# Optimization experiments

Measured on AMD Instinct MI355X. Metric: run time of the kernel, lower is better.

The kernel has to match this reference:

```python
import jax, jax.numpy as jnp
import numpy as np

N, IN_DIM, HID, HEAD = 32768, 512, 512, 4
E = 524288


def setup_inputs() -> dict:
    key = jax.random.key(0)
    ks = jax.random.split(key, 12)
    s_in = 1.0 / np.sqrt(IN_DIM)
    s_h = 1.0 / np.sqrt(HID)
    s_c = 1.0 / np.sqrt(HID * HEAD)
    s_f = 1.0 / np.sqrt(HID * 2)
    return {
        "x": jax.random.normal(ks[0], (N, IN_DIM), jnp.float32),
        "inter_h": jax.random.normal(ks[1], (N, IN_DIM), jnp.float32),
        "edge_index": jax.random.randint(ks[2], (2, E), 0, N, jnp.int64),
        "batch": jnp.zeros((N,), jnp.int64),
        # per-head projection weights stored [HEAD, in, out] (x @ W)
        "Wq": jax.random.uniform(ks[3], (HEAD, IN_DIM, HID), jnp.float32, -s_in, s_in),
        "Wk": jax.random.uniform(ks[4], (HEAD, IN_DIM, HID), jnp.float32, -s_in, s_in),
        "Wv": jax.random.uniform(ks[5], (HEAD, IN_DIM, HID), jnp.float32, -s_in, s_in),
        "Wc": jax.random.uniform(ks[6], (HID * HEAD, HID), jnp.float32, -s_c, s_c),
        "W1": jax.random.uniform(ks[7], (HID, HID * 2), jnp.float32, -s_h, s_h),
        "b1": jax.random.uniform(ks[8], (HID * 2,), jnp.float32, -s_h, s_h),
        "W2": jax.random.uniform(ks[9], (HID * 2, HID), jnp.float32, -s_f, s_f),
        "b2": jax.random.uniform(ks[10], (HID,), jnp.float32, -s_f, s_f),
        "ln_g": jnp.ones((HID,), jnp.float32),
        "ln_b": jnp.zeros((HID,), jnp.float32),
    }


def _layernorm(h, g, b, eps=1e-5):
    mu = jnp.mean(h, axis=-1, keepdims=True)
    var = jnp.mean(jnp.square(h - mu), axis=-1, keepdims=True)
    return (h - mu) * jax.lax.rsqrt(var + eps) * g + b


def reference(x, inter_h, edge_index, batch, Wq, Wk, Wv, Wc, W1, b1, W2, b2, ln_g, ln_b):
    # edge_index and batch are unused by the original forward.
    q = jnp.einsum("ni,hio->nho", x, Wq)        # [N, H, D]
    k = jnp.einsum("ni,hio->nho", inter_h, Wk)  # [N, H, D]
    v = jnp.einsum("ni,hio->nho", x, Wv)        # [N, H, D]
    scale = 1.0 / jnp.sqrt(jnp.float32(HID))
    att = jnp.sum(q * k, axis=-1) * scale       # [N, H]
    alpha = jax.nn.softmax(att, axis=0)         # softmax over nodes (dim 0)
    tp = v * alpha[:, :, None]                  # [N, H, D]
    mo = tp.reshape(tp.shape[0], HEAD * HID)    # head-major concat, matches torch.cat(dim=1)
    mo = mo @ Wc                                # [N, D]
    h1 = _layernorm(mo + x, ln_g, ln_b)
    ff = jnp.maximum(h1 @ W1 + b1, 0.0) @ W2 + b2
    return _layernorm(ff + h1, ln_g, ln_b)
```

## Files before the change

kernel.cpp:

```cpp
#include <hip/hip_runtime.h>

typedef unsigned short u16;
typedef short short8 __attribute__((ext_vector_type(8)));
typedef unsigned short ushort8 __attribute__((ext_vector_type(8)));
typedef float f32x4 __attribute__((ext_vector_type(4)));

#define NN 32768L

__device__ __forceinline__ u16 f2bf(float f) {
  unsigned u = __float_as_uint(f);
  u += 0x7FFFu + ((u >> 16) & 1u);
  return (u16)(u >> 16);
}
__device__ __forceinline__ float bf2f(u16 u) {
  return __uint_as_float(((unsigned)u) << 16);
}

__global__ __launch_bounds__(256) void fill_f32_k(float* __restrict__ out, long n, float v) {
  long i = (long)blockIdx.x * 256 + threadIdx.x;
  if (i < n) out[i] = v;
}

__global__ __launch_bounds__(256) void cast_bf16_k(const float* __restrict__ in,
                                                   u16* __restrict__ out, long n) {
  long i = ((long)blockIdx.x * 256 + threadIdx.x) * 8;
  if (i >= n) return;
  const float4* p = (const float4*)(in + i);
  float4 a = p[0], b = p[1];
  ushort8 r;
  r[0] = f2bf(a.x); r[1] = f2bf(a.y); r[2] = f2bf(a.z); r[3] = f2bf(a.w);
  r[4] = f2bf(b.x); r[5] = f2bf(b.y); r[6] = f2bf(b.z); r[7] = f2bf(b.w);
  *(ushort8*)(out + i) = r;
}

__global__ __launch_bounds__(256) void transpose_cast(const float* __restrict__ in,
                                                      u16* __restrict__ out, int R, int C) {
  __shared__ float t[32][33];
  int c0 = blockIdx.x * 32, r0 = blockIdx.y * 32;
  int tx = threadIdx.x, ty = threadIdx.y;
#pragma unroll
  for (int j = 0; j < 32; j += 8)
    t[ty + j][tx] = in[(long)(r0 + ty + j) * C + c0 + tx];
  __syncthreads();
#pragma unroll
  for (int j = 0; j < 32; j += 8)
    out[(long)(c0 + ty + j) * R + r0 + tx] = f2bf(t[tx][ty + j]);
}

template <int EPI>
__global__ __launch_bounds__(256) void gemm_bt(const u16* __restrict__ A,
                                               const u16* __restrict__ Bt,
                                               u16* __restrict__ C, int K,
                                               int lda, int ldb, int ldc,
                                               long sA, long sB, long sC,
                                               const float* __restrict__ ep0) {
  __shared__ u16 As[4096];
  __shared__ u16 Bs[4096];
  const int tid = threadIdx.x;
  const int wid = tid >> 6, lane = tid & 63;
  const int bx = blockIdx.x, by = blockIdx.y, bz = blockIdx.z;
  const u16* Ab = A + bz * sA + (long)by * 128 * lda;
  const u16* Bb = Bt + bz * sB + (long)bx * 128 * ldb;
  const int e0 = tid * 8;
  const int ar = e0 >> 5, ac = e0 & 31;
  const int r15 = lane & 15, kg = lane >> 4;
  const int wrow = (wid >> 1) * 64, wcol = (wid & 1) * 64;

  f32x4 acc[4][4];
  const f32x4 z4 = {0.f, 0.f, 0.f, 0.f};
#pragma unroll
  for (int mi = 0; mi < 4; ++mi)
#pragma unroll
    for (int ni = 0; ni < 4; ++ni) acc[mi][ni] = z4;

  for (int k0 = 0; k0 < K; k0 += 32) {
    short8 a0 = *(const short8*)(Ab + (long)ar * lda + k0 + ac);
    short8 a1 = *(const short8*)(Ab + (long)(ar + 64) * lda + k0 + ac);
    short8 b0 = *(const short8*)(Bb + (long)ar * ldb + k0 + ac);
    short8 b1 = *(const short8*)(Bb + (long)(ar + 64) * ldb + k0 + ac);
    *(short8*)(As + e0) = a0;
    *(short8*)(As + e0 + 2048) = a1;
    *(short8*)(Bs + e0) = b0;
    *(short8*)(Bs + e0 + 2048) = b1;
    __syncthreads();
    short8 af[4], bfr[4];
#pragma unroll
    for (int mi = 0; mi < 4; ++mi)
      af[mi] = *(const short8*)(As + (wrow + mi * 16 + r15) * 32 + kg * 8);
#pragma unroll
    for (int ni = 0; ni < 4; ++ni)
      bfr[ni] = *(const short8*)(Bs + (wcol + ni * 16 + r15) * 32 + kg * 8);
#pragma unroll
    for (int mi = 0; mi < 4; ++mi)
#pragma unroll
      for (int ni = 0; ni < 4; ++ni)
        acc[mi][ni] =
            __builtin_amdgcn_mfma_f32_16x16x32_bf16(af[mi], bfr[ni], acc[mi][ni], 0, 0, 0);
    __syncthreads();
  }

  u16* Cp = C + bz * sC;
  const long crow0 = (long)by * 128 + wrow;
  const int ccol0 = bx * 128 + wcol;
#pragma unroll
  for (int mi = 0; mi < 4; ++mi) {
#pragma unroll
    for (int ni = 0; ni < 4; ++ni) {
      const int gc = ccol0 + ni * 16 + r15;
#pragma unroll
      for (int r = 0; r < 4; ++r) {
        const long gr = crow0 + mi * 16 + kg * 4 + r;
        float v = acc[mi][ni][r];
        if (EPI == 1) { v += ep0[gc]; v = fmaxf(v, 0.f); }
        if (EPI == 2) { v += ep0[gc]; }
        Cp[gr * ldc + gc] = f2bf(v);
      }
    }
  }
}

__global__ __launch_bounds__(256) void att_dot_k(const float* __restrict__ x,
                                                 const u16* __restrict__ zb,
                                                 float* __restrict__ att) {
  int wid = threadIdx.x >> 6, lane = threadIdx.x & 63;
  long n = (long)blockIdx.x * 4 + wid;
  const float4* xp = (const float4*)(x + n * 512 + lane * 8);
  float4 x0 = xp[0], x1 = xp[1];
  float xf[8] = {x0.x, x0.y, x0.z, x0.w, x1.x, x1.y, x1.z, x1.w};
  const float scale = 0.044194173824159216f;
#pragma unroll
  for (int h = 0; h < 4; ++h) {
    ushort8 zv = *(const ushort8*)(zb + n * 2048 + h * 512 + lane * 8);
    float s = 0.f;
#pragma unroll
    for (int j = 0; j < 8; ++j) s += xf[j] * bf2f(zv[j]);
#pragma unroll
    for (int o = 32; o; o >>= 1) s += __shfl_xor(s, o);
    if (lane == 0) att[n * 4 + h] = s * scale;
  }
}

__global__ __launch_bounds__(1024) void softmax_k(const float* __restrict__ att,
                                                  float* __restrict__ alpha) {
  int h = blockIdx.x;
  int tid = threadIdx.x;
  __shared__ float red[16];
  float lm = -1e30f;
  for (long i = tid; i < NN; i += 1024) lm = fmaxf(lm, att[i * 4 + h]);
#pragma unroll
  for (int o = 32; o; o >>= 1) lm = fmaxf(lm, __shfl_xor(lm, o));
  if ((tid & 63) == 0) red[tid >> 6] = lm;
  __syncthreads();
  float gm = red[0];
  for (int i = 1; i < 16; ++i) gm = fmaxf(gm, red[i]);
  __syncthreads();
  float ls = 0.f;
  for (long i = tid; i < NN; i += 1024) ls += __expf(att[i * 4 + h] - gm);
#pragma unroll
  for (int o = 32; o; o >>= 1) ls += __shfl_xor(ls, o);
  if ((tid & 63) == 0) red[tid >> 6] = ls;
  __syncthreads();
  float gs = 0.f;
  for (int i = 0; i < 16; ++i) gs += red[i];
  float inv = 1.0f / gs;
  for (long i = tid; i < NN; i += 1024)
    alpha[i * 4 + h] = __expf(att[i * 4 + h] - gm) * inv;
}

__global__ __launch_bounds__(256) void ascale_k(const float* __restrict__ x,
                                                const float* __restrict__ alpha,
                                                u16* __restrict__ out, long row0) {
  long e = ((long)blockIdx.x * 256 + threadIdx.x) * 8;
  long r = e >> 11;
  int c = (int)(e & 2047);
  int h = c >> 9;
  float al = alpha[(row0 + r) * 4 + h];
  const float4* xp = (const float4*)(x + (row0 + r) * 512 + (c & 511));
  float4 x0 = xp[0], x1 = xp[1];
  ushort8 o;
  o[0] = f2bf(al * x0.x); o[1] = f2bf(al * x0.y);
  o[2] = f2bf(al * x0.z); o[3] = f2bf(al * x0.w);
  o[4] = f2bf(al * x1.x); o[5] = f2bf(al * x1.y);
  o[6] = f2bf(al * x1.z); o[7] = f2bf(al * x1.w);
  *(ushort8*)(out + e) = o;
}

template <int RBF, int OUTF>
__global__ __launch_bounds__(256) void ln_k(const u16* __restrict__ a,
                                            const void* __restrict__ resid,
                                            const float* __restrict__ g,
                                            const float* __restrict__ b,
                                            void* __restrict__ out) {
  int wid = threadIdx.x >> 6, lane = threadIdx.x & 63;
  long row = (long)blockIdx.x * 4 + wid;
  ushort8 av = *(const ushort8*)(a + row * 512 + lane * 8);
  float v[8];
  if (RBF) {
    ushort8 rv = *(const ushort8*)((const u16*)resid + row * 512 + lane * 8);
#pragma unroll
    for (int j = 0; j < 8; ++j) v[j] = bf2f(av[j]) + bf2f(rv[j]);
  } else {
    const float4* rp = (const float4*)((const float*)resid + row * 512 + lane * 8);
    float4 r0 = rp[0], r1 = rp[1];
    float rr[8] = {r0.x, r0.y, r0.z, r0.w, r1.x, r1.y, r1.z, r1.w};
#pragma unroll
    for (int j = 0; j < 8; ++j) v[j] = bf2f(av[j]) + rr[j];
  }
  float s = 0.f, q = 0.f;
#pragma unroll
  for (int j = 0; j < 8; ++j) { s += v[j]; q += v[j] * v[j]; }
#pragma unroll
  for (int o = 32; o; o >>= 1) { s += __shfl_xor(s, o); q += __shfl_xor(q, o); }
  float mu = s * (1.0f / 512.0f);
  float var = q * (1.0f / 512.0f) - mu * mu;
  float rs = rsqrtf(var + 1e-5f);
  const float4* gp = (const float4*)(g + lane * 8);
  const float4* bp = (const float4*)(b + lane * 8);
  float4 g0 = gp[0], g1 = gp[1], b0 = bp[0], b1 = bp[1];
  float gg[8] = {g0.x, g0.y, g0.z, g0.w, g1.x, g1.y, g1.z, g1.w};
  float bb[8] = {b0.x, b0.y, b0.z, b0.w, b1.x, b1.y, b1.z, b1.w};
  float o_[8];
#pragma unroll
  for (int j = 0; j < 8; ++j) o_[j] = (v[j] - mu) * rs * gg[j] + bb[j];
  if (OUTF) {
    float4 q0 = {o_[0], o_[1], o_[2], o_[3]}, q1 = {o_[4], o_[5], o_[6], o_[7]};
    float4* op = (float4*)((float*)out + row * 512 + lane * 8);
    op[0] = q0;
    op[1] = q1;
  } else {
    ushort8 r;
#pragma unroll
    for (int j = 0; j < 8; ++j) r[j] = f2bf(o_[j]);
    *(ushort8*)((u16*)out + row * 512 + lane * 8) = r;
  }
}

extern "C" void kernel_launch(void* const* d_in, const int* in_sizes, int n_in,
                              void* d_out, int out_size, void* d_ws, size_t ws_size,
                              hipStream_t stream) {
  static const int EXPS[14] = {16777216, 16777216, 1048576, 32768, 1048576, 1048576,
                               1048576,  1048576,  524288,  1024,  524288,  512,
                               512,      512};
  float sv = 0.f;
  if (n_in != 14) {
    sv = 390.f;
  } else {
    for (int i = 0; i < 14; ++i)
      if (in_sizes[i] != EXPS[i]) { sv = 200.f + 10.f * i; break; }
  }
  if (sv == 0.f && out_size != 16777216) sv = 400.f;
  if (sv == 0.f && ws_size < 116391936UL) sv = 500.f + (float)(ws_size >> 24);
  if (sv != 0.f) {
    fill_f32_k<<<65536, 256, 0, stream>>>((float*)d_out, 16777216L, sv);
    return;
  }

  const float* x   = (const float*)d_in[0];
  const float* ih  = (const float*)d_in[1];
  const float* Wq  = (const float*)d_in[4];
  const float* Wk  = (const float*)d_in[5];
  const float* Wv  = (const float*)d_in[6];
  const float* Wc  = (const float*)d_in[7];
  const float* W1  = (const float*)d_in[8];
  const float* b1  = (const float*)d_in[9];
  const float* W2  = (const float*)d_in[10];
  const float* b2  = (const float*)d_in[11];
  const float* lng = (const float*)d_in[12];
  const float* lnb = (const float*)d_in[13];

  char* w = (char*)d_ws;
  u16* yb   = (u16*)(w + 0L);
  u16* apc  = (u16*)(w + 0L);
  u16* f1c  = (u16*)(w + 0L);
  u16* zc   = (u16*)(w + 33554432L);
  u16* moc  = (u16*)(w + 33554432L);
  u16* g2   = (u16*)(w + 33554432L);
  u16* h1   = (u16*)(w + 67108864L);
  char* wb  = w + 100663296L;
  u16* Wqb  = (u16*)(wb + 0L);
  u16* Wkb  = (u16*)(wb + 2097152L);
  u16* Wvb  = (u16*)(wb + 4194304L);
  u16* Wct  = (u16*)(wb + 6291456L);
  u16* Mcat = (u16*)(wb + 8388608L);
  u16* Pt   = (u16*)(wb + 10485760L);
  u16* W1t  = (u16*)(wb + 12582912L);
  u16* W2t  = (u16*)(wb + 13631488L);
  float* att   = (float*)(wb + 14680064L);
  float* alpha = (float*)(wb + 15204352L);

  dim3 b256(256);

  cast_bf16_k<<<8192, b256, 0, stream>>>(ih, yb, 16777216L);
  cast_bf16_k<<<512, b256, 0, stream>>>(Wq, Wqb, 1048576L);
  cast_bf16_k<<<512, b256, 0, stream>>>(Wk, Wkb, 1048576L);
  cast_bf16_k<<<512, b256, 0, stream>>>(Wv, Wvb, 1048576L);
  transpose_cast<<<dim3(16, 64), dim3(32, 8), 0, stream>>>(Wc, Wct, 2048, 512);
  transpose_cast<<<dim3(32, 16), dim3(32, 8), 0, stream>>>(W1, W1t, 512, 1024);
  transpose_cast<<<dim3(16, 32), dim3(32, 8), 0, stream>>>(W2, W2t, 1024, 512);

  gemm_bt<0><<<dim3(4, 4, 4), b256, 0, stream>>>(Wqb, Wkb, Mcat, 512, 512, 512, 512,
                                                 262144L, 262144L, 262144L, nullptr);
  gemm_bt<0><<<dim3(4, 4, 4), b256, 0, stream>>>(Wct, Wvb, Pt, 512, 2048, 512, 2048,
                                                 512L, 262144L, 512L, nullptr);

  for (int c = 0; c < 8; ++c) {
    long r0 = (long)c * 4096;
    gemm_bt<0><<<dim3(16, 32), b256, 0, stream>>>(yb + r0 * 512, Mcat, zc, 512,
                                                  512, 512, 2048, 0L, 0L, 0L, nullptr);
    att_dot_k<<<1024, b256, 0, stream>>>(x + r0 * 512, zc, att + r0 * 4);
  }
  softmax_k<<<4, 1024, 0, stream>>>(att, alpha);

  for (int c = 0; c < 4; ++c) {
    long r0 = (long)c * 8192;
    ascale_k<<<8192, b256, 0, stream>>>(x, alpha, apc, r0);
    gemm_bt<0><<<dim3(4, 64), b256, 0, stream>>>(apc, Pt, moc, 2048,
                                                 2048, 2048, 512, 0L, 0L, 0L, nullptr);
    ln_k<0, 0><<<2048, b256, 0, stream>>>(moc, x + r0 * 512, lng, lnb, h1 + r0 * 512);
  }

  for (int c = 0; c < 4; ++c) {
    long r0 = (long)c * 8192;
    gemm_bt<1><<<dim3(8, 64), b256, 0, stream>>>(h1 + r0 * 512, W1t, f1c, 512,
                                                 512, 512, 1024, 0L, 0L, 0L, b1);
    gemm_bt<2><<<dim3(4, 64), b256, 0, stream>>>(f1c, W2t, g2 + r0 * 512, 1024,
                                                 1024, 1024, 512, 0L, 0L, 0L, b2);
  }

  ln_k<1, 1><<<8192, b256, 0, stream>>>(g2, h1, lng, lnb, d_out);
}
```

Baseline: 932.7 us.

## Fuse attention dot and alpha scaling into GEMMs, drop row chunking

The attention-score dot product is folded into the epilogue of the z GEMM, which reduces across lanes and accumulates per-head scores with atomicAdd, so the bf16 z intermediate is never written out. The alpha-times-x bf16 operand is built on the fly in the A-load of the Wc GEMM, which removes the separate ascale kernel and its buffer. The chunked launch loops are replaced by single full-size launches, and the workspace is enlarged to hold full-size intermediates. In exchange the code adds atomics, a zero-fill of the score buffer, and fp32 x loads and conversion inside the GEMM inner loop, which may slow that loop.

After: 764.5 us. 1.22x faster.

```diff
diff --git a/kernel.cpp b/kernel.cpp
--- a/kernel.cpp
+++ b/kernel.cpp
@@ -47,13 +47,15 @@
     out[(long)(c0 + ty + j) * R + r0 + tx] = f2bf(t[tx][ty + j]);
 }
 
-template <int EPI>
+template <int EPI, int ASRC>
 __global__ __launch_bounds__(256) void gemm_bt(const u16* __restrict__ A,
                                                const u16* __restrict__ Bt,
-                                               u16* __restrict__ C, int K,
+                                               void* __restrict__ C, int K,
                                                int lda, int ldb, int ldc,
                                                long sA, long sB, long sC,
-                                               const float* __restrict__ ep0) {
+                                               const float* __restrict__ ep0,
+                                               const float* __restrict__ xf,
+                                               const float* __restrict__ alf) {
   __shared__ u16 As[4096];
   __shared__ u16 Bs[4096];
   const int tid = threadIdx.x;
@@ -74,8 +76,27 @@
     for (int ni = 0; ni < 4; ++ni) acc[mi][ni] = z4;
 
   for (int k0 = 0; k0 < K; k0 += 32) {
-    short8 a0 = *(const short8*)(Ab + (long)ar * lda + k0 + ac);
-    short8 a1 = *(const short8*)(Ab + (long)(ar + 64) * lda + k0 + ac);
+    short8 a0, a1;
+    if (ASRC == 0) {
+      a0 = *(const short8*)(Ab + (long)ar * lda + k0 + ac);
+      a1 = *(const short8*)(Ab + (long)(ar + 64) * lda + k0 + ac);
+    } else {
+      const int hh = (k0 + ac) >> 9, cc = (k0 + ac) & 511;
+      const long r0a = (long)by * 128 + ar;
+      const float al0 = alf[r0a * 4 + hh];
+      const float al1 = alf[(r0a + 64) * 4 + hh];
+      const float4* p0 = (const float4*)(xf + r0a * 512 + cc);
+      const float4* p1 = (const float4*)(xf + (r0a + 64) * 512 + cc);
+      float4 u0 = p0[0], u1 = p0[1], v0 = p1[0], v1 = p1[1];
+      a0[0] = (short)f2bf(al0 * u0.x); a0[1] = (short)f2bf(al0 * u0.y);
+      a0[2] = (short)f2bf(al0 * u0.z); a0[3] = (short)f2bf(al0 * u0.w);
+      a0[4] = (short)f2bf(al0 * u1.x); a0[5] = (short)f2bf(al0 * u1.y);
+      a0[6] = (short)f2bf(al0 * u1.z); a0[7] = (short)f2bf(al0 * u1.w);
+      a1[0] = (short)f2bf(al1 * v0.x); a1[1] = (short)f2bf(al1 * v0.y);
+      a1[2] = (short)f2bf(al1 * v0.z); a1[3] = (short)f2bf(al1 * v0.w);
+      a1[4] = (short)f2bf(al1 * v1.x); a1[5] = (short)f2bf(al1 * v1.y);
+      a1[6] = (short)f2bf(al1 * v1.z); a1[7] = (short)f2bf(al1 * v1.w);
+    }
     short8 b0 = *(const short8*)(Bb + (long)ar * ldb + k0 + ac);
     short8 b1 = *(const short8*)(Bb + (long)(ar + 64) * ldb + k0 + ac);
     *(short8*)(As + e0) = a0;
@@ -99,9 +120,32 @@
     __syncthreads();
   }
 
-  u16* Cp = C + bz * sC;
   const long crow0 = (long)by * 128 + wrow;
   const int ccol0 = bx * 128 + wcol;
+
+  if (EPI == 3) {
+    const int hh = ccol0 >> 9;
+    const int cb = (ccol0 & 511) + r15;
+    float* att = (float*)C;
+    const float scale = 0.044194173824159216f;
+#pragma unroll
+    for (int mi = 0; mi < 4; ++mi) {
+#pragma unroll
+      for (int r = 0; r < 4; ++r) {
+        const long gr = crow0 + mi * 16 + kg * 4 + r;
+        float p = 0.f;
+#pragma unroll
+        for (int ni = 0; ni < 4; ++ni)
+          p += acc[mi][ni][r] * xf[gr * 512 + cb + ni * 16];
+        p += __shfl_xor(p, 1); p += __shfl_xor(p, 2);
+        p += __shfl_xor(p, 4); p += __shfl_xor(p, 8);
+        if (r15 == 0) atomicAdd(att + gr * 4 + hh, p * scale);
+      }
+    }
+    return;
+  }
+
+  u16* Cp = (u16*)C + bz * sC;
 #pragma unroll
   for (int mi = 0; mi < 4; ++mi) {
 #pragma unroll
@@ -119,27 +163,6 @@
   }
 }
 
-__global__ __launch_bounds__(256) void att_dot_k(const float* __restrict__ x,
-                                                 const u16* __restrict__ zb,
-                                                 float* __restrict__ att) {
-  int wid = threadIdx.x >> 6, lane = threadIdx.x & 63;
-  long n = (long)blockIdx.x * 4 + wid;
-  const float4* xp = (const float4*)(x + n * 512 + lane * 8);
-  float4 x0 = xp[0], x1 = xp[1];
-  float xf[8] = {x0.x, x0.y, x0.z, x0.w, x1.x, x1.y, x1.z, x1.w};
-  const float scale = 0.044194173824159216f;
-#pragma unroll
-  for (int h = 0; h < 4; ++h) {
-    ushort8 zv = *(const ushort8*)(zb + n * 2048 + h * 512 + lane * 8);
-    float s = 0.f;
-#pragma unroll
-    for (int j = 0; j < 8; ++j) s += xf[j] * bf2f(zv[j]);
-#pragma unroll
-    for (int o = 32; o; o >>= 1) s += __shfl_xor(s, o);
-    if (lane == 0) att[n * 4 + h] = s * scale;
-  }
-}
-
 __global__ __launch_bounds__(1024) void softmax_k(const float* __restrict__ att,
                                                   float* __restrict__ alpha) {
   int h = blockIdx.x;
@@ -165,24 +188,6 @@
   float inv = 1.0f / gs;
   for (long i = tid; i < NN; i += 1024)
     alpha[i * 4 + h] = __expf(att[i * 4 + h] - gm) * inv;
-}
-
-__global__ __launch_bounds__(256) void ascale_k(const float* __restrict__ x,
-                                                const float* __restrict__ alpha,
-                                                u16* __restrict__ out, long row0) {
-  long e = ((long)blockIdx.x * 256 + threadIdx.x) * 8;
-  long r = e >> 11;
-  int c = (int)(e & 2047);
-  int h = c >> 9;
-  float al = alpha[(row0 + r) * 4 + h];
-  const float4* xp = (const float4*)(x + (row0 + r) * 512 + (c & 511));
-  float4 x0 = xp[0], x1 = xp[1];
-  ushort8 o;
-  o[0] = f2bf(al * x0.x); o[1] = f2bf(al * x0.y);
-  o[2] = f2bf(al * x0.z); o[3] = f2bf(al * x0.w);
-  o[4] = f2bf(al * x1.x); o[5] = f2bf(al * x1.y);
-  o[6] = f2bf(al * x1.z); o[7] = f2bf(al * x1.w);
-  *(ushort8*)(out + e) = o;
 }
 
 template <int RBF, int OUTF>
@@ -249,7 +254,7 @@
       if (in_sizes[i] != EXPS[i]) { sv = 200.f + 10.f * i; break; }
   }
   if (sv == 0.f && out_size != 16777216) sv = 400.f;
-  if (sv == 0.f && ws_size < 116391936UL) sv = 500.f + (float)(ws_size >> 24);
+  if (sv == 0.f && ws_size < 149946368UL) sv = 500.f + (float)(ws_size >> 24);
   if (sv != 0.f) {
     fill_f32_k<<<65536, 256, 0, stream>>>((float*)d_out, 16777216L, sv);
     return;
@@ -270,13 +275,11 @@
 
   char* w = (char*)d_ws;
   u16* yb   = (u16*)(w + 0L);
-  u16* apc  = (u16*)(w + 0L);
-  u16* f1c  = (u16*)(w + 0L);
-  u16* zc   = (u16*)(w + 33554432L);
-  u16* moc  = (u16*)(w + 33554432L);
-  u16* g2   = (u16*)(w + 33554432L);
-  u16* h1   = (u16*)(w + 67108864L);
-  char* wb  = w + 100663296L;
+  u16* f1   = (u16*)(w + 0L);
+  u16* moc  = (u16*)(w + 67108864L);
+  u16* g2   = (u16*)(w + 67108864L);
+  u16* h1   = (u16*)(w + 100663296L);
+  char* wb  = w + 134217728L;
   u16* Wqb  = (u16*)(wb + 0L);
   u16* Wkb  = (u16*)(wb + 2097152L);
   u16* Wvb  = (u16*)(wb + 4194304L);
@@ -297,35 +300,28 @@
   transpose_cast<<<dim3(16, 64), dim3(32, 8), 0, stream>>>(Wc, Wct, 2048, 512);
   transpose_cast<<<dim3(32, 16), dim3(32, 8), 0, stream>>>(W1, W1t, 512, 1024);
   transpose_cast<<<dim3(16, 32), dim3(32, 8), 0, stream>>>(W2, W2t, 1024, 512);
-
-  gemm_bt<0><<<dim3(4, 4, 4), b256, 0, stream>>>(Wqb, Wkb, Mcat, 512, 512, 512, 512,
-                                                 262144L, 262144L, 262144L, nullptr);
-  gemm_bt<0><<<dim3(4, 4, 4), b256, 0, stream>>>(Wct, Wvb, Pt, 512, 2048, 512, 2048,
-                                                 512L, 262144L, 512L, nullptr);
-
-  for (int c = 0; c < 8; ++c) {
-    long r0 = (long)c * 4096;
-    gemm_bt<0><<<dim3(16, 32), b256, 0, stream>>>(yb + r0 * 512, Mcat, zc, 512,
-                                                  512, 512, 2048, 0L, 0L, 0L, nullptr);
-    att_dot_k<<<1024, b256, 0, stream>>>(x + r0 * 512, zc, att + r0 * 4);
-  }
+  fill_f32_k<<<512, b256, 0, stream>>>(att, 131072L, 0.f);
+
+  gemm_bt<0, 0><<<dim3(4, 4, 4), b256, 0, stream>>>(
+      Wqb, Wkb, Mcat, 512, 512, 512, 512, 262144L, 262144L, 262144L,
+      nullptr, nullptr, nullptr);
+  gemm_bt<0, 0><<<dim3(4, 4, 4), b256, 0, stream>>>(
+      Wct, Wvb, Pt, 512, 2048, 512, 2048, 512L, 262144L, 512L,
+      nullptr, nullptr, nullptr);
+
+  gemm_bt<3, 0><<<dim3(16, 256), b256, 0, stream>>>(
+      yb, Mcat, att, 512, 512, 512, 0, 0L, 0L, 0L, nullptr, x, nullptr);
   softmax_k<<<4, 1024, 0, stream>>>(att, alpha);
 
-  for (int c = 0; c < 4; ++c) {
-    long r0 = (long)c * 8192;
-    ascale_k<<<8192, b256, 0, stream>>>(x, alpha, apc, r0);
-    gemm_bt<0><<<dim3(4, 64), b256, 0, stream>>>(apc, Pt, moc, 2048,
-                                                 2048, 2048, 512, 0L, 0L, 0L, nullptr);
-    ln_k<0, 0><<<2048, b256, 0, stream>>>(moc, x + r0 * 512, lng, lnb, h1 + r0 * 512);
-  }
-
-  for (int c = 0; c < 4; ++c) {
-    long r0 = (long)c * 8192;
-    gemm_bt<1><<<dim3(8, 64), b256, 0, stream>>>(h1 + r0 * 512, W1t, f1c, 512,
-                                                 512, 512, 1024, 0L, 0L, 0L, b1);
-    gemm_bt<2><<<dim3(4, 64), b256, 0, stream>>>(f1c, W2t, g2 + r0 * 512, 1024,
-                                                 1024, 1024, 512, 0L, 0L, 0L, b2);
-  }
+  gemm_bt<0, 1><<<dim3(4, 256), b256, 0, stream>>>(
+      nullptr, Pt, moc, 2048, 0, 2048, 512, 0L, 0L, 0L, nullptr, x, alpha);
+
+  ln_k<0, 0><<<8192, b256, 0, stream>>>(moc, x, lng, lnb, h1);
+
+  gemm_bt<1, 0><<<dim3(8, 256), b256, 0, stream>>>(
+      h1, W1t, f1, 512, 512, 512, 1024, 0L, 0L, 0L, b1, nullptr, nullptr);
+  gemm_bt<2, 0><<<dim3(4, 256), b256, 0, stream>>>(
+      f1, W2t, g2, 1024, 1024, 1024, 512, 0L, 0L, 0L, b2, nullptr, nullptr);
 
   ln_k<1, 1><<<8192, b256, 0, stream>>>(g2, h1, lng, lnb, d_out);
 }
```
